# Kernel tuning notes

Hardware: AMD Instinct MI355X
Metric: run time of the kernel (lower is better)

## Reference

```python
import jax, jax.numpy as jnp
import numpy as np

ROI, P = 28, 7          # ROI window on feature map; output grid 7x7 -> 4x4 bins
BIN = ROI // P
C, CLASSES = 64, 2      # channels after vgg features[:2]; n classes
H = W = 512
N_ROI = 2000
D_FC = 4096


def setup_inputs() -> dict:
    key = jax.random.key(0)
    k = jax.random.split(key, 8)
    s = 0.02
    return {
        "img": jax.random.normal(k[0], (3, H, W), jnp.float32),
        "regions": jax.random.randint(k[1], (N_ROI, 2), 0, H - ROI, jnp.int32),
        "conv_w": jax.random.normal(k[2], (C, 3, 3, 3), jnp.float32) * s,
        "conv_b": jnp.zeros((C,), jnp.float32),
        "fc1_w": jax.random.normal(k[3], (D_FC, C * P * P), jnp.float32) * s,
        "fc1_b": jnp.zeros((D_FC,), jnp.float32),
        "fc2_w": jax.random.normal(k[4], (D_FC, D_FC), jnp.float32) * s,
        "fc2_b": jnp.zeros((D_FC,), jnp.float32),
        "cls_w": jax.random.normal(k[5], (CLASSES, D_FC), jnp.float32) * s,
        "cls_b": jnp.zeros((CLASSES,), jnp.float32),
        "bbox_w": jax.random.normal(k[6], (CLASSES * 4, D_FC), jnp.float32) * s,
        "bbox_b": jnp.zeros((CLASSES * 4,), jnp.float32),
    }


def reference(img, regions, conv_w, conv_b, fc1_w, fc1_b,
              fc2_w, fc2_b, cls_w, cls_b, bbox_w, bbox_b):
    # conv trunk: vgg16.features[:2] = Conv2d(3,64,3,pad=1) + ReLU
    fmap = jax.lax.conv_general_dilated(
        img[None], conv_w, window_strides=(1, 1), padding="SAME",
        dimension_numbers=("NCHW", "OIHW", "NCHW"))[0]
    fmap = jax.nn.relu(fmap + conv_b[:, None, None])        # [C, H, W]

    # per-region crop (irregular gather), vectorized over regions
    def crop(rc):
        return jax.lax.dynamic_slice(fmap, (0, rc[0], rc[1]), (C, ROI, ROI))
    rois = jax.vmap(crop)(regions)                          # [N, C, ROI, ROI]

    # RoI max pooling: divide ROIxROI window into PxP grid, max each bin
    pooled = rois.reshape(N_ROI, C, P, BIN, P, BIN).max(axis=(3, 5))  # [N,C,P,P]
    feat = pooled.reshape(N_ROI, C * P * P)

    # vgg classifier[:-1] (Dropout = identity at inference)
    feat = jax.nn.relu(feat @ fc1_w.T + fc1_b)
    feat = jax.nn.relu(feat @ fc2_w.T + fc2_b)              # [N, 4096]

    cls_logits = feat @ cls_w.T + cls_b                     # [N, CLASSES]
    loc_bbox = feat @ bbox_w.T + bbox_b                     # [N, CLASSES*4]
    return (cls_logits, loc_bbox)
```

## Files before the change

kernel.cpp:

```cpp
#include <hip/hip_runtime.h>

typedef unsigned short u16;
typedef unsigned int u32;
using bf16x8 = __attribute__((ext_vector_type(8))) short;
using f32x4  = __attribute__((ext_vector_type(4))) float;

__device__ __forceinline__ u16 f2bf(float f) {
  u32 u = __float_as_uint(f);
  return (u16)((u + 0x7FFFu + ((u >> 16) & 1u)) >> 16);
}
__device__ __forceinline__ float bf2f(u16 h) {
  return __uint_as_float(((u32)h) << 16);
}

__global__ __launch_bounds__(256) void conv3x3_relu_k(
    const float* __restrict__ img, const float* __restrict__ w,
    const float* __restrict__ bias, u16* __restrict__ fmap) {
  int p = blockIdx.x * 256 + threadIdx.x;
  int y = p >> 9, x = p & 511;
  float v[27];
#pragma unroll
  for (int ci = 0; ci < 3; ++ci)
#pragma unroll
    for (int ky = 0; ky < 3; ++ky)
#pragma unroll
      for (int kx = 0; kx < 3; ++kx) {
        int yy = y + ky - 1, xx = x + kx - 1;
        bool ok = (yy >= 0) && (yy < 512) && (xx >= 0) && (xx < 512);
        v[(ci * 3 + ky) * 3 + kx] = ok ? img[ci * 262144 + yy * 512 + xx] : 0.f;
      }
  float acc[64];
#pragma unroll
  for (int co = 0; co < 64; ++co) {
    float s = bias[co];
#pragma unroll
    for (int q = 0; q < 27; ++q) s = fmaf(w[co * 27 + q], v[q], s);
    acc[co] = fmaxf(s, 0.f);
  }
  uint4* dst = (uint4*)((u32*)fmap + (size_t)p * 32);
#pragma unroll
  for (int q = 0; q < 8; ++q) {
    uint4 d;
    d.x = (u32)f2bf(acc[8 * q + 0]) | ((u32)f2bf(acc[8 * q + 1]) << 16);
    d.y = (u32)f2bf(acc[8 * q + 2]) | ((u32)f2bf(acc[8 * q + 3]) << 16);
    d.z = (u32)f2bf(acc[8 * q + 4]) | ((u32)f2bf(acc[8 * q + 5]) << 16);
    d.w = (u32)f2bf(acc[8 * q + 6]) | ((u32)f2bf(acc[8 * q + 7]) << 16);
    dst[q] = d;
  }
}

__global__ __launch_bounds__(256) void roipool_k(
    const u16* __restrict__ fmap, const int* __restrict__ regions,
    u16* __restrict__ feat) {
  int n = blockIdx.x, t = threadIdx.x;
  uint4* fdst = (uint4*)(feat + (size_t)n * 3136);
  if (n >= 2000) {
    uint4 z; z.x = z.y = z.z = z.w = 0u;
    fdst[t % 392] = z;
    int t2 = t + 256; if (t2 < 392) fdst[t2] = z;
    if (t < 392) fdst[t] = z;
    return;
  }
  int r0 = regions[2 * n], c0 = regions[2 * n + 1];
  __shared__ uint2 rows_u2[1792];
  __shared__ uint4 frow4[392];
  u16* rows = (u16*)rows_u2;
  u16* frow = (u16*)frow4;
  for (int py = 0; py < 7; ++py) {
#pragma unroll
    for (int q = 0; q < 7; ++q) {
      int cid = t + q * 256;
      int i = cid / 448, rem = cid % 448;
      int xo = rem >> 4, c4 = (rem & 15) << 2;
      int yy = r0 + py * 4 + i, xx = c0 + xo;
      rows_u2[cid] = *(const uint2*)(fmap + (((size_t)(yy * 512 + xx)) << 6) + c4);
    }
    __syncthreads();
#pragma unroll
    for (int h = 0; h < 2; ++h) {
      int o = t + h * 256;
      if (o < 448) {
        int c = o & 63, px = o >> 6;
        float best = -3.0e38f;
#pragma unroll
        for (int i = 0; i < 4; ++i)
#pragma unroll
          for (int j = 0; j < 4; ++j)
            best = fmaxf(best, bf2f(rows[(i * 28 + px * 4 + j) * 64 + c]));
        frow[c * 49 + py * 7 + px] = f2bf(best);
      }
    }
    __syncthreads();
  }
  if (t < 392) fdst[t] = frow4[t];
  int t2 = t + 256;
  if (t2 < 392) fdst[t2] = frow4[t2];
}

__global__ __launch_bounds__(256) void f2bf_k(const float* __restrict__ in,
                                              u16* __restrict__ out, int n4) {
  int idx = blockIdx.x * 256 + threadIdx.x;
  int stride = gridDim.x * 256;
  for (int i = idx; i < n4; i += stride) {
    float4 v = ((const float4*)in)[i];
    uint2 o;
    o.x = (u32)f2bf(v.x) | ((u32)f2bf(v.y) << 16);
    o.y = (u32)f2bf(v.z) | ((u32)f2bf(v.w) << 16);
    ((uint2*)out)[i] = o;
  }
}

__global__ __launch_bounds__(512, 2) void gemm8_bt_relu_k(
    const u16* __restrict__ A, const u16* __restrict__ B,
    const float* __restrict__ bias, u16* __restrict__ C, int N, int K) {
  __shared__ uint4 lds4[9216];
  char* ldsb = (char*)lds4;
  const int t = threadIdx.x;
  const int lane = t & 63, wv = t >> 6;
  const int wm = wv >> 2, wn = wv & 3;

  int bid = blockIdx.x;
  int swz = ((bid & 7) << 5) | (bid >> 3);
  const int nb = swz >> 4, mb = swz & 15;
  const int m0 = mb * 128, n0 = nb * 256;

  const u16* __restrict__ Ab = A + (size_t)m0 * K;
  const u16* __restrict__ Bb = B + (size_t)n0 * K;

  const int srow = t >> 3;
  const int sslot = (t & 7) ^ (srow & 7);
  const u16* pA0 = Ab + (size_t)srow * K + sslot * 8;
  const u16* pA1 = pA0 + (size_t)64 * K;
  const u16* pB0 = Bb + (size_t)srow * K + sslot * 8;
  const u16* pB1 = pB0 + (size_t)64 * K;
  const u16* pB2 = pB0 + (size_t)128 * K;
  const u16* pB3 = pB0 + (size_t)192 * K;
  const int dof = t * 16;

#define G2L(src, ldst)                                                        \
  __builtin_amdgcn_global_load_lds(                                          \
      (const __attribute__((address_space(1))) void*)(src),                  \
      (__attribute__((address_space(3))) void*)(ldst), 16, 0, 0)

  const int rA = wm * 64 + (lane & 15);
  const int rB = wn * 64 + (lane & 15);
  const int sl = lane >> 4;
#define LOFF(r, slot) (((r) << 7) + ((((slot) ^ ((r) & 7))) << 4))

  f32x4 acc[4][4] = {};
  bf16x8 afr[4][2], bfr[4][2];

  const int NT = K >> 6;
  {
    char* A0 = ldsb; char* B0 = A0 + 16384;
    char* A1 = ldsb + 49152; char* B1 = A1 + 16384;
    G2L(pA0, A0 + dof); G2L(pA1, A0 + 8192 + dof);
    G2L(pB0, B0 + dof); G2L(pB1, B0 + 8192 + dof);
    G2L(pB2, B0 + 16384 + dof); G2L(pB3, B0 + 24576 + dof);
    G2L(pA0 + 64, A1 + dof); G2L(pA1 + 64, A1 + 8192 + dof);
    G2L(pB0 + 64, B1 + dof); G2L(pB1 + 64, B1 + 8192 + dof);
    G2L(pB2 + 64, B1 + 16384 + dof); G2L(pB3 + 64, B1 + 24576 + dof);
  }
  asm volatile("s_waitcnt vmcnt(6)" ::: "memory");
  __builtin_amdgcn_s_barrier();

  int cb = 0;
  for (int tt = 0; tt < NT; ++tt) {
    const int pb = (cb + 2 >= 3) ? cb - 1 : cb + 2;
    const bool pf = (tt + 2) < NT;
    char* Acur = ldsb + cb * 49152; char* Bcur = Acur + 16384;
    char* Apf  = ldsb + pb * 49152; char* Bpf  = Apf + 16384;
    const int kof = (tt + 2) << 6;

    if (pf) {
      G2L(pA0 + kof, Apf + dof);
      G2L(pA1 + kof, Apf + 8192 + dof);
      G2L(pB0 + kof, Bpf + dof);
      G2L(pB1 + kof, Bpf + 8192 + dof);
      G2L(pB2 + kof, Bpf + 16384 + dof);
      G2L(pB3 + kof, Bpf + 24576 + dof);
    }
    __builtin_amdgcn_sched_barrier(0);
    __builtin_amdgcn_s_setprio(1);
#pragma unroll
    for (int j = 0; j < 4; ++j) {
      bfr[j][0] = *(const bf16x8*)(Bcur + LOFF(rB + j * 16, sl));
      bfr[j][1] = *(const bf16x8*)(Bcur + LOFF(rB + j * 16, 4 + sl));
    }
#pragma unroll
    for (int i = 0; i < 4; ++i) {
      afr[i][0] = *(const bf16x8*)(Acur + LOFF(rA + i * 16, sl));
      afr[i][1] = *(const bf16x8*)(Acur + LOFF(rA + i * 16, 4 + sl));
    }
#pragma unroll
    for (int i = 0; i < 4; ++i)
#pragma unroll
      for (int j = 0; j < 4; ++j) {
        acc[i][j] = __builtin_amdgcn_mfma_f32_16x16x32_bf16(afr[i][0], bfr[j][0], acc[i][j], 0, 0, 0);
        acc[i][j] = __builtin_amdgcn_mfma_f32_16x16x32_bf16(afr[i][1], bfr[j][1], acc[i][j], 0, 0, 0);
      }
    __builtin_amdgcn_s_setprio(0);
    if (pf) {
      asm volatile("s_waitcnt vmcnt(6)" ::: "memory");
    } else if (tt + 1 < NT) {
      asm volatile("s_waitcnt vmcnt(0)" ::: "memory");
    }
    __builtin_amdgcn_s_barrier();
    cb = (cb == 2) ? 0 : cb + 1;
  }
#undef G2L
#undef LOFF

  float bv[4];
#pragma unroll
  for (int j = 0; j < 4; ++j) bv[j] = bias[n0 + wn * 64 + j * 16 + (lane & 15)];
#pragma unroll
  for (int i = 0; i < 4; ++i)
#pragma unroll
    for (int j = 0; j < 4; ++j) {
      int cg = n0 + wn * 64 + j * 16 + (lane & 15);
#pragma unroll
      for (int r = 0; r < 4; ++r) {
        int rg = m0 + wm * 64 + i * 16 + (lane >> 4) * 4 + r;
        float v = fmaxf(acc[i][j][r] + bv[j], 0.f);
        C[(size_t)rg * N + cg] = f2bf(v);
      }
    }
}

__global__ __launch_bounds__(256) void heads_k(
    const u16* __restrict__ h2, const float* __restrict__ cw,
    const float* __restrict__ cb, const float* __restrict__ bw,
    const float* __restrict__ bb, float* __restrict__ out) {
  int m = blockIdx.x, t = threadIdx.x;
  const u16* hrow = h2 + (size_t)m * 4096;
  float p[10];
#pragma unroll
  for (int j = 0; j < 10; ++j) p[j] = 0.f;
  for (int k = t; k < 4096; k += 256) {
    float v = bf2f(hrow[k]);
    p[0] = fmaf(v, cw[k], p[0]);
    p[1] = fmaf(v, cw[4096 + k], p[1]);
#pragma unroll
    for (int j = 0; j < 8; ++j) p[2 + j] = fmaf(v, bw[j * 4096 + k], p[2 + j]);
  }
#pragma unroll
  for (int j = 0; j < 10; ++j)
#pragma unroll
    for (int off = 32; off > 0; off >>= 1) p[j] += __shfl_down(p[j], off);
  __shared__ float red[4][10];
  int lane = t & 63, wv = t >> 6;
  if (lane == 0) {
#pragma unroll
    for (int j = 0; j < 10; ++j) red[wv][j] = p[j];
  }
  __syncthreads();
  if (t < 10) {
    float s = red[0][t] + red[1][t] + red[2][t] + red[3][t];
    s += (t < 2) ? cb[t] : bb[t - 2];
    if (t < 2) out[m * 2 + t] = s;
    else out[4000 + m * 8 + (t - 2)] = s;
  }
}

extern "C" void kernel_launch(void* const* d_in, const int* in_sizes, int n_in,
                              void* d_out, int out_size, void* d_ws, size_t ws_size,
                              hipStream_t stream) {
  const float* img    = (const float*)d_in[0];
  const int*   regions= (const int*)d_in[1];
  const float* conv_w = (const float*)d_in[2];
  const float* conv_b = (const float*)d_in[3];
  const float* fc1_w  = (const float*)d_in[4];
  const float* fc1_b  = (const float*)d_in[5];
  const float* fc2_w  = (const float*)d_in[6];
  const float* fc2_b  = (const float*)d_in[7];
  const float* cls_w  = (const float*)d_in[8];
  const float* cls_b  = (const float*)d_in[9];
  const float* bbox_w = (const float*)d_in[10];
  const float* bbox_b = (const float*)d_in[11];
  float* out = (float*)d_out;

  char* ws = (char*)d_ws;
  u16* fmap = (u16*)(ws);
  u16* feat = (u16*)(ws + 33554432);
  u16* w1b  = (u16*)(ws + 46399488);
  u16* w2b  = (u16*)(ws + 72089600);
  u16* h1   = (u16*)(ws);
  u16* h2   = (u16*)(ws + 16777216);

  conv3x3_relu_k<<<1024, 256, 0, stream>>>(img, conv_w, conv_b, fmap);
  roipool_k<<<2048, 256, 0, stream>>>(fmap, regions, feat);
  f2bf_k<<<2048, 256, 0, stream>>>(fc1_w, w1b, 4096 * 3136 / 4);
  f2bf_k<<<2048, 256, 0, stream>>>(fc2_w, w2b, 4096 * 4096 / 4);
  gemm8_bt_relu_k<<<256, 512, 0, stream>>>(feat, w1b, fc1_b, h1, 4096, 3136);
  gemm8_bt_relu_k<<<256, 512, 0, stream>>>(h1, w2b, fc2_b, h2, 4096, 4096);
  heads_k<<<2000, 256, 0, stream>>>(h2, cls_w, cls_b, bbox_w, bbox_b, out);
}
```

Baseline: 229.3 us.

## Precompute vertical 4-row max map so RoI pooling needs only four loads per bin

Adds a pass that computes a sliding 4-row vertical max over the whole feature map, using unsigned bf16 max, which is valid because ReLU output is non-negative. RoI pooling then reads four horizontally adjacent vectors per bin instead of 16 rows through shared memory. This removes redundant per-ROI gather traffic, since ROIs overlap heavily, at the cost of an extra full-map read and write pass and a relaid-out workspace. The vmax kernel launches only 128 blocks, so that pass has low parallelism.

```diff
diff --git a/kernel.cpp b/kernel.cpp
--- a/kernel.cpp
+++ b/kernel.cpp
@@ -4,6 +4,7 @@
 typedef unsigned int u32;
 using bf16x8 = __attribute__((ext_vector_type(8))) short;
 using f32x4  = __attribute__((ext_vector_type(4))) float;
+using ushort8 = __attribute__((ext_vector_type(8))) unsigned short;
 
 __device__ __forceinline__ u16 f2bf(float f) {
   u32 u = __float_as_uint(f);
@@ -11,6 +12,9 @@
 }
 __device__ __forceinline__ float bf2f(u16 h) {
   return __uint_as_float(((u32)h) << 16);
+}
+__device__ __forceinline__ ushort8 umax8(ushort8 a, ushort8 b) {
+  return __builtin_elementwise_max(a, b);
 }
 
 __global__ __launch_bounds__(256) void conv3x3_relu_k(
@@ -49,52 +53,51 @@
   }
 }
 
-__global__ __launch_bounds__(256) void roipool_k(
-    const u16* __restrict__ fmap, const int* __restrict__ regions,
+__global__ __launch_bounds__(256) void vmax_k(
+    const u16* __restrict__ fmap, u16* __restrict__ M1) {
+  int g = blockIdx.x * 256 + threadIdx.x;
+  int cg = g & 7, x = (g >> 3) & 511, ych = g >> 12;
+  int y0 = ych * 64;
+  ushort8 h0, h1, h2;
+  for (int i = 0; i < 67; ++i) {
+    int yy = y0 + i; if (yy > 511) yy = 511;
+    ushort8 r = *(const ushort8*)(fmap + (((size_t)(yy * 512 + x)) << 6) + cg * 8);
+    if (i >= 3) {
+      ushort8 m = umax8(umax8(h0, h1), umax8(h2, r));
+      *(ushort8*)(M1 + (((size_t)((y0 + i - 3) * 512 + x)) << 6) + cg * 8) = m;
+    }
+    h0 = h1; h1 = h2; h2 = r;
+  }
+}
+
+__global__ __launch_bounds__(256) void roipool2_k(
+    const u16* __restrict__ M1, const int* __restrict__ regions,
     u16* __restrict__ feat) {
   int n = blockIdx.x, t = threadIdx.x;
   uint4* fdst = (uint4*)(feat + (size_t)n * 3136);
   if (n >= 2000) {
     uint4 z; z.x = z.y = z.z = z.w = 0u;
-    fdst[t % 392] = z;
-    int t2 = t + 256; if (t2 < 392) fdst[t2] = z;
-    if (t < 392) fdst[t] = z;
+    for (int w = t; w < 392; w += 256) fdst[w] = z;
     return;
   }
+  __shared__ u16 frow[3136];
   int r0 = regions[2 * n], c0 = regions[2 * n + 1];
-  __shared__ uint2 rows_u2[1792];
-  __shared__ uint4 frow4[392];
-  u16* rows = (u16*)rows_u2;
-  u16* frow = (u16*)frow4;
-  for (int py = 0; py < 7; ++py) {
-#pragma unroll
-    for (int q = 0; q < 7; ++q) {
-      int cid = t + q * 256;
-      int i = cid / 448, rem = cid % 448;
-      int xo = rem >> 4, c4 = (rem & 15) << 2;
-      int yy = r0 + py * 4 + i, xx = c0 + xo;
-      rows_u2[cid] = *(const uint2*)(fmap + (((size_t)(yy * 512 + xx)) << 6) + c4);
-    }
-    __syncthreads();
-#pragma unroll
-    for (int h = 0; h < 2; ++h) {
-      int o = t + h * 256;
-      if (o < 448) {
-        int c = o & 63, px = o >> 6;
-        float best = -3.0e38f;
-#pragma unroll
-        for (int i = 0; i < 4; ++i)
-#pragma unroll
-          for (int j = 0; j < 4; ++j)
-            best = fmaxf(best, bf2f(rows[(i * 28 + px * 4 + j) * 64 + c]));
-        frow[c * 49 + py * 7 + px] = f2bf(best);
-      }
-    }
-    __syncthreads();
-  }
-  if (t < 392) fdst[t] = frow4[t];
-  int t2 = t + 256;
-  if (t2 < 392) fdst[t2] = frow4[t2];
+  for (int w = t; w < 392; w += 256) {
+    int bin = w >> 3, cg = w & 7;
+    int py = bin / 7, px = bin % 7;
+    int y = r0 + py * 4, xb = c0 + px * 4;
+    const u16* base = M1 + (((size_t)(y * 512 + xb)) << 6) + cg * 8;
+    ushort8 a = *(const ushort8*)(base);
+    ushort8 b = *(const ushort8*)(base + 64);
+    ushort8 c = *(const ushort8*)(base + 128);
+    ushort8 d = *(const ushort8*)(base + 192);
+    ushort8 m = umax8(umax8(a, b), umax8(c, d));
+#pragma unroll
+    for (int k = 0; k < 8; ++k) frow[(cg * 8 + k) * 49 + bin] = m[k];
+  }
+  __syncthreads();
+  const uint4* fsrc = (const uint4*)frow;
+  for (int w = t; w < 392; w += 256) fdst[w] = fsrc[w];
 }
 
 __global__ __launch_bounds__(256) void f2bf_k(const float* __restrict__ in,
@@ -282,14 +285,16 @@
 
   char* ws = (char*)d_ws;
   u16* fmap = (u16*)(ws);
-  u16* feat = (u16*)(ws + 33554432);
-  u16* w1b  = (u16*)(ws + 46399488);
-  u16* w2b  = (u16*)(ws + 72089600);
   u16* h1   = (u16*)(ws);
   u16* h2   = (u16*)(ws + 16777216);
+  u16* M1   = (u16*)(ws + 33554432);
+  u16* w2b  = (u16*)(ws + 33554432);
+  u16* feat = (u16*)(ws + 67108864);
+  u16* w1b  = (u16*)(ws + 79953920);
 
   conv3x3_relu_k<<<1024, 256, 0, stream>>>(img, conv_w, conv_b, fmap);
-  roipool_k<<<2048, 256, 0, stream>>>(fmap, regions, feat);
+  vmax_k<<<128, 256, 0, stream>>>(fmap, M1);
+  roipool2_k<<<2048, 256, 0, stream>>>(M1, regions, feat);
   f2bf_k<<<2048, 256, 0, stream>>>(fc1_w, w1b, 4096 * 3136 / 4);
   f2bf_k<<<2048, 256, 0, stream>>>(fc2_w, w2b, 4096 * 4096 / 4);
   gemm8_bt_relu_k<<<256, 512, 0, stream>>>(feat, w1b, fc1_b, h1, 4096, 3136);
```

Result: no change. 224.9 us (-1.9%).
